# Optimization experiments

Hardware: AMD Instinct MI355X
Metric: run time of the kernel (lower is better)

Reference implementation:

```python
import jax, jax.numpy as jnp
import numpy as np

N_FFT = 4096
HOP = 1024
HALF = N_FFT // 2  # 2048; also number of freq bins is HALF+1 = 2049


def _make_kernels():
    # Periodic hann window, matching torch.hann_window(N) default (periodic=True)
    n = np.arange(N_FFT, dtype=np.float32)
    window = 0.5 * (1.0 - np.cos(2.0 * np.pi * n / N_FFT))
    freqs = np.arange(HALF + 1, dtype=np.float32)[:, None]  # [K,1]
    omega = 2.0 * np.pi * freqs * n[None, :] / N_FFT        # [K, n_fft]
    scale = np.float32(1.0 / np.sqrt(N_FFT))                # normalized=True
    cos_k = (np.cos(omega) * window[None, :] * scale).astype(np.float32)
    sin_k = (-np.sin(omega) * window[None, :] * scale).astype(np.float32)
    return jnp.asarray(cos_k), jnp.asarray(sin_k)


def setup_inputs() -> dict:
    key = jax.random.key(0)
    x = jax.random.normal(key, (32, 1, 441000), dtype=jnp.float32)
    cos_kernel, sin_kernel = _make_kernels()  # each [2049, 4096]
    return {"x": x, "cos_kernel": cos_kernel, "sin_kernel": sin_kernel}


def reference(x, cos_kernel, sin_kernel):
    # center=True: reflect-pad half_n_fft on each side of the time axis
    xp = jnp.pad(x, ((0, 0), (0, 0), (HALF, HALF)), mode='reflect')  # [B,1,L]
    L = xp.shape[-1]
    num_frames = (L - N_FFT) // HOP + 1
    # Frame extraction (equivalent to stride-HOP conv1d with width-N_FFT kernels)
    idx = HOP * jnp.arange(num_frames)[:, None] + jnp.arange(N_FFT)[None, :]  # [F, n_fft]
    frames = xp[:, 0, :][:, idx]  # [B, F, n_fft]
    real = jnp.einsum('bfn,kn->bkf', frames, cos_kernel)  # [B, 2049, F]
    imag = jnp.einsum('bfn,kn->bkf', frames, sin_kernel)  # [B, 2049, F]
    return jnp.stack((real, imag), axis=-1)  # [B, 2049, F, 2]
```

## Files before the change

kernel.cpp:

```cpp
#include <hip/hip_runtime.h>
#include <math.h>

#define NFFT  4096
#define MHALF 2048
#define HOPSZ 1024
#define LX    441000
#define NB    32
#define NF    431
#define NK    2049
#define NFPB  8
#define FBLK  54
#define NWG3  (NB * FBLK)
#define CH3   (NWG3 / 8)

#define SW(A) ((A) ^ (((A) >> 4) & 0xF))
#define WAVESYNC() do { asm volatile("s_waitcnt lgkmcnt(0)" ::: "memory"); \
                        __builtin_amdgcn_sched_barrier(0); } while (0)

typedef __fp16 half2v __attribute__((ext_vector_type(2)));

__device__ __forceinline__ float2 cadd(float2 a, float2 b){ return make_float2(a.x+b.x, a.y+b.y); }
__device__ __forceinline__ float2 csub(float2 a, float2 b){ return make_float2(a.x-b.x, a.y-b.y); }
__device__ __forceinline__ float2 cmul(float2 a, float2 b){
  return make_float2(fmaf(a.x, b.x, -(a.y*b.y)), fmaf(a.x, b.y, a.y*b.x));
}
#define STH(ptr, idx, v) (ptr)[idx] = __builtin_amdgcn_cvt_pkrtz((v).x, (v).y)
__device__ __forceinline__ float2 ldh(const half2v* __restrict__ X, int idx) {
  half2v h = X[idx];
  return make_float2((float)h.x, (float)h.y);
}

__global__ void stft_init(float* __restrict__ ws) {
  int i = blockIdx.x * blockDim.x + threadIdx.x;
  const double PI = 3.14159265358979323846;
  if (i < 4096) {
    double w = 0.5 * (1.0 - cos(2.0 * PI * (double)i / 4096.0)) * (1.0 / 64.0);
    ws[i] = (float)w;
  }
  if (i < 1024) {
    double a = -2.0 * PI * (double)i / 2048.0;
    ws[4096 + 2 * i]     = (float)cos(a);
    ws[4096 + 2 * i + 1] = (float)sin(a);
  }
  if (i < 2049) {
    double a = -2.0 * PI * (double)i / 4096.0;
    ws[6144 + 2 * i]     = (float)cos(a);
    ws[6144 + 2 * i + 1] = (float)sin(a);
  }
}

template<int S>
__device__ __forceinline__ void bf8(half2v* __restrict__ X,
                                    const float2* __restrict__ twg,
                                    int j, const float2* a) {
  const int q = j & (S - 1);
  const int t = j - q;
  float2 t0 = cadd(a[0], a[4]), t1 = csub(a[0], a[4]);
  float2 t2 = cadd(a[2], a[6]), t3 = csub(a[2], a[6]);
  float2 t4 = cadd(a[1], a[5]), t5 = csub(a[1], a[5]);
  float2 t6 = cadd(a[3], a[7]), t7 = csub(a[3], a[7]);

  const float K = 0.70710678118654752f;
  float2 wt5  = make_float2(K * (t5.x + t5.y), K * (t5.y - t5.x));
  float2 w3t7 = make_float2(K * (t7.y - t7.x), -K * (t7.x + t7.y));
  float2 wt7  = make_float2(K * (t7.x + t7.y), K * (t7.y - t7.x));
  float2 w3t5 = make_float2(K * (t5.y - t5.x), -K * (t5.x + t5.y));

  float2 e0 = cadd(t0, t2), e1 = csub(t0, t2);
  float2 f0 = cadd(t4, t6), f1 = csub(t4, t6);
  float2 B0 = cadd(e0, f0);
  float2 B4 = csub(e0, f0);
  float2 B2 = make_float2(e1.x + f1.y, e1.y - f1.x);
  float2 B6 = make_float2(e1.x - f1.y, e1.y + f1.x);
  float2 g0 = make_float2(t1.x + t3.y, t1.y - t3.x);
  float2 g1 = make_float2(t1.x - t3.y, t1.y + t3.x);
  float2 h0 = cadd(wt5, w3t7);
  float2 h1 = cadd(wt7, w3t5);
  float2 B1 = cadd(g0, h0);
  float2 B5 = csub(g0, h0);
  float2 B3 = cadd(g1, h1);
  float2 B7 = csub(g1, h1);

  float2 w1 = twg[t];
  float2 w2 = cmul(w1, w1);
  float2 w3 = cmul(w2, w1);
  float2 w4 = cmul(w2, w2);
  float2 w5 = cmul(w3, w2);
  float2 w6 = cmul(w3, w3);
  float2 w7 = cmul(w4, w3);

  const int o = q + 8 * t;
  STH(X, SW(o), B0);
  { float2 v = cmul(w1, B1); STH(X, SW(o + S),     v); }
  { float2 v = cmul(w2, B2); STH(X, SW(o + 2 * S), v); }
  { float2 v = cmul(w3, B3); STH(X, SW(o + 3 * S), v); }
  { float2 v = cmul(w4, B4); STH(X, SW(o + 4 * S), v); }
  { float2 v = cmul(w5, B5); STH(X, SW(o + 5 * S), v); }
  { float2 v = cmul(w6, B6); STH(X, SW(o + 6 * S), v); }
  { float2 v = cmul(w7, B7); STH(X, SW(o + 7 * S), v); }
}

__global__ __launch_bounds__(512) void stft_fft(const float* __restrict__ x,
                                                const float* __restrict__ ws,
                                                float* __restrict__ out) {
  __shared__ half2v fbuf[NFPB * 2048];

  const int tid = threadIdx.x;
  const int wid = (blockIdx.x & 7) * CH3 + (blockIdx.x >> 3);
  const int b  = wid / FBLK;
  const int fb = wid - b * FBLK;
  const int f0 = fb * NFPB;
  const int wv = tid >> 6;
  const int l  = tid & 63;
  const int f  = f0 + wv;

  const float*  win  = ws;
  const float2* winv = (const float2*)ws;
  const float2* twg  = (const float2*)(ws + 4096);
  const float2* tw4  = (const float2*)(ws + 6144);
  const float* xb = x + (size_t)b * LX;

  if (f < NF) {
    half2v* __restrict__ sl = &fbuf[wv * 2048];
    const int base = f * HOPSZ - MHALF;

    float2 a[4][8];
    if (base >= 0 && base + NFFT <= LX) {
      const float2* xv = (const float2*)(xb + base);
#pragma unroll
      for (int r = 0; r < 4; ++r) {
        const int j = l + (r << 6);
#pragma unroll
        for (int m = 0; m < 8; ++m) {
          const int idx = j + (m << 8);
          float2 v = xv[idx];
          float2 w = winv[idx];
          a[r][m] = make_float2(v.x * w.x, v.y * w.y);
        }
      }
    } else {
#pragma unroll
      for (int r = 0; r < 4; ++r) {
        const int j = l + (r << 6);
#pragma unroll
        for (int m = 0; m < 8; ++m) {
          const int idx = j + (m << 8);
          int s0 = base + 2 * idx;
          int s1 = s0 + 1;
          s0 = (s0 < 0) ? -s0 : ((s0 >= LX) ? (2 * LX - 2 - s0) : s0);
          s1 = (s1 < 0) ? -s1 : ((s1 >= LX) ? (2 * LX - 2 - s1) : s1);
          a[r][m] = make_float2(xb[s0] * win[2 * idx], xb[s1] * win[2 * idx + 1]);
        }
      }
    }
#pragma unroll
    for (int r = 0; r < 4; ++r) bf8<1>(sl, twg, l + (r << 6), a[r]);
    WAVESYNC();

#pragma unroll
    for (int r = 0; r < 4; ++r) {
      const int j = l + (r << 6);
#pragma unroll
      for (int m = 0; m < 8; ++m) a[r][m] = ldh(sl, SW(j + (m << 8)));
    }
    WAVESYNC();
#pragma unroll
    for (int r = 0; r < 4; ++r) bf8<8>(sl, twg, l + (r << 6), a[r]);
    WAVESYNC();

#pragma unroll
    for (int r = 0; r < 4; ++r) {
      const int j = l + (r << 6);
#pragma unroll
      for (int m = 0; m < 8; ++m) a[r][m] = ldh(sl, SW(j + (m << 8)));
    }
    WAVESYNC();
#pragma unroll
    for (int r = 0; r < 4; ++r) bf8<64>(sl, twg, l + (r << 6), a[r]);
    WAVESYNC();

#pragma unroll
    for (int r = 0; r < 8; ++r) {
      const int j = l + (r << 6);
      float2 c0 = ldh(sl, SW(j));
      float2 c1 = ldh(sl, SW(j + 512));
      float2 c2 = ldh(sl, SW(j + 1024));
      float2 c3 = ldh(sl, SW(j + 1536));
      float2 e0 = cadd(c0, c2), e1 = csub(c0, c2);
      float2 o0 = cadd(c1, c3), o1 = csub(c1, c3);
      { float2 v = cadd(e0, o0);                          STH(sl, SW(j),        v); }
      { float2 v = make_float2(e1.x + o1.y, e1.y - o1.x); STH(sl, SW(j + 512),  v); }
      { float2 v = csub(e0, o0);                          STH(sl, SW(j + 1024), v); }
      { float2 v = make_float2(e1.x - o1.y, e1.y + o1.x); STH(sl, SW(j + 1536), v); }
    }
  }
  __syncthreads();

  float2* __restrict__ op = (float2*)out;
  const size_t obB = (size_t)b * NK * NF;
  const int s  = tid & 7;
  const int kk = tid >> 3;
  const int fS = f0 + s;
  const bool act = (fS < NF);
  const half2v* __restrict__ sl = &fbuf[s * 2048];
#pragma unroll 4
  for (int it = 0; it < 32; ++it) {
    const int k  = kk + (it << 6);
    const int km = (2048 - k) & 2047;
    float2 zk = ldh(sl, SW(k));
    float2 zm = ldh(sl, SW(km));
    float xex = 0.5f * (zk.x + zm.x);
    float xey = 0.5f * (zk.y - zm.y);
    float xox = 0.5f * (zk.y + zm.y);
    float xoy = 0.5f * (zm.x - zk.x);
    float2 w = tw4[k];
    if (act)
      op[obB + (size_t)k * NF + fS] =
          make_float2(xex + w.x * xox - w.y * xoy, xey + w.x * xoy + w.y * xox);
  }
  if (tid < 8 && act) {
    float2 z0 = ldh(sl, 0);
    op[obB + (size_t)2048 * NF + fS] = make_float2(z0.x - z0.y, 0.0f);
  }
}

extern "C" void kernel_launch(void* const* d_in, const int* in_sizes, int n_in,
                              void* d_out, int out_size, void* d_ws, size_t ws_size,
                              hipStream_t stream) {
  const float* x = (const float*)d_in[0];
  float* ws = (float*)d_ws;
  float* out = (float*)d_out;
  stft_init<<<16, 256, 0, stream>>>(ws);
  stft_fft<<<NWG3, 512, 0, stream>>>(x, ws, out);
}
```

Baseline: 140.4 us.

## Merge last FFT stages into a register radix-32 pass and exploit conjugate symmetry

Replaces the final radix-8 LDS pass and the radix-4 pass with a single in-register radix-32 step: 32 values are loaded once, a radix-4 butterfly runs, then radix-8 DFTs with compile-time twiddles. This removes one LDS round trip and its wave syncs. The post-processing loop now uses the Hermitian symmetry of the real-FFT split, so each iteration writes bins k and 2048-k and the loop count is halved. A per-wave XOR offset is also added to the LDS addressing, likely to spread bank conflicts across waves. The radix-32 pass needs more registers, and the special-case handling of bins 0, 1024 and 2048 changes.

```diff
diff --git a/kernel.cpp b/kernel.cpp
--- a/kernel.cpp
+++ b/kernel.cpp
@@ -30,6 +30,29 @@
   return make_float2((float)h.x, (float)h.y);
 }
 
+constexpr float W32C[22] = {
+  1.0f, 0.98078528040323f, 0.92387953251129f, 0.83146961230255f, 0.70710678118655f,
+  0.55557023301960f, 0.38268343236509f, 0.19509032201613f, 0.0f, -0.19509032201613f,
+  -0.38268343236509f, -0.55557023301960f, -0.70710678118655f, -0.83146961230255f,
+  -0.92387953251129f, -0.98078528040323f, -1.0f, -0.98078528040323f,
+  -0.92387953251129f, -0.83146961230255f, -0.70710678118655f, -0.55557023301960f };
+constexpr float W32S[22] = {
+  0.0f, 0.19509032201613f, 0.38268343236509f, 0.55557023301960f, 0.70710678118655f,
+  0.83146961230255f, 0.92387953251129f, 0.98078528040323f, 1.0f, 0.98078528040323f,
+  0.92387953251129f, 0.83146961230255f, 0.70710678118655f, 0.55557023301960f,
+  0.38268343236509f, 0.19509032201613f, 0.0f, -0.19509032201613f,
+  -0.38268343236509f, -0.55557023301960f, -0.70710678118655f, -0.83146961230255f };
+
+template<int N> __device__ __forceinline__ float2 w32m(float2 z) {
+  if constexpr (N == 0) { return z; }
+  else if constexpr (N == 8) { return make_float2(z.y, -z.x); }
+  else {
+    constexpr float c = W32C[N];
+    constexpr float s = W32S[N];
+    return make_float2(fmaf(z.x, c, z.y * s), fmaf(z.y, c, -(z.x * s)));
+  }
+}
+
 __global__ void stft_init(float* __restrict__ ws) {
   int i = blockIdx.x * blockDim.x + threadIdx.x;
   const double PI = 3.14159265358979323846;
@@ -49,38 +72,40 @@
   }
 }
 
-template<int S>
-__device__ __forceinline__ void bf8(half2v* __restrict__ X,
-                                    const float2* __restrict__ twg,
-                                    int j, const float2* a) {
-  const int q = j & (S - 1);
-  const int t = j - q;
+__device__ __forceinline__ void dft8(const float2* a, float2* B) {
   float2 t0 = cadd(a[0], a[4]), t1 = csub(a[0], a[4]);
   float2 t2 = cadd(a[2], a[6]), t3 = csub(a[2], a[6]);
   float2 t4 = cadd(a[1], a[5]), t5 = csub(a[1], a[5]);
   float2 t6 = cadd(a[3], a[7]), t7 = csub(a[3], a[7]);
-
   const float K = 0.70710678118654752f;
   float2 wt5  = make_float2(K * (t5.x + t5.y), K * (t5.y - t5.x));
   float2 w3t7 = make_float2(K * (t7.y - t7.x), -K * (t7.x + t7.y));
   float2 wt7  = make_float2(K * (t7.x + t7.y), K * (t7.y - t7.x));
   float2 w3t5 = make_float2(K * (t5.y - t5.x), -K * (t5.x + t5.y));
-
   float2 e0 = cadd(t0, t2), e1 = csub(t0, t2);
   float2 f0 = cadd(t4, t6), f1 = csub(t4, t6);
-  float2 B0 = cadd(e0, f0);
-  float2 B4 = csub(e0, f0);
-  float2 B2 = make_float2(e1.x + f1.y, e1.y - f1.x);
-  float2 B6 = make_float2(e1.x - f1.y, e1.y + f1.x);
+  B[0] = cadd(e0, f0);
+  B[4] = csub(e0, f0);
+  B[2] = make_float2(e1.x + f1.y, e1.y - f1.x);
+  B[6] = make_float2(e1.x - f1.y, e1.y + f1.x);
   float2 g0 = make_float2(t1.x + t3.y, t1.y - t3.x);
   float2 g1 = make_float2(t1.x - t3.y, t1.y + t3.x);
   float2 h0 = cadd(wt5, w3t7);
   float2 h1 = cadd(wt7, w3t5);
-  float2 B1 = cadd(g0, h0);
-  float2 B5 = csub(g0, h0);
-  float2 B3 = cadd(g1, h1);
-  float2 B7 = csub(g1, h1);
-
+  B[1] = cadd(g0, h0);
+  B[5] = csub(g0, h0);
+  B[3] = cadd(g1, h1);
+  B[7] = csub(g1, h1);
+}
+
+template<int S>
+__device__ __forceinline__ void bf8(half2v* __restrict__ X, int sxor,
+                                    const float2* __restrict__ twg,
+                                    int j, const float2* a) {
+  const int q = j & (S - 1);
+  const int t = j - q;
+  float2 B[8];
+  dft8(a, B);
   float2 w1 = twg[t];
   float2 w2 = cmul(w1, w1);
   float2 w3 = cmul(w2, w1);
@@ -88,17 +113,37 @@
   float2 w5 = cmul(w3, w2);
   float2 w6 = cmul(w3, w3);
   float2 w7 = cmul(w4, w3);
-
   const int o = q + 8 * t;
-  STH(X, SW(o), B0);
-  { float2 v = cmul(w1, B1); STH(X, SW(o + S),     v); }
-  { float2 v = cmul(w2, B2); STH(X, SW(o + 2 * S), v); }
-  { float2 v = cmul(w3, B3); STH(X, SW(o + 3 * S), v); }
-  { float2 v = cmul(w4, B4); STH(X, SW(o + 4 * S), v); }
-  { float2 v = cmul(w5, B5); STH(X, SW(o + 5 * S), v); }
-  { float2 v = cmul(w6, B6); STH(X, SW(o + 6 * S), v); }
-  { float2 v = cmul(w7, B7); STH(X, SW(o + 7 * S), v); }
-}
+  STH(X, SW(o) ^ sxor, B[0]);
+  { float2 v = cmul(w1, B[1]); STH(X, SW(o + S)     ^ sxor, v); }
+  { float2 v = cmul(w2, B[2]); STH(X, SW(o + 2 * S) ^ sxor, v); }
+  { float2 v = cmul(w3, B[3]); STH(X, SW(o + 3 * S) ^ sxor, v); }
+  { float2 v = cmul(w4, B[4]); STH(X, SW(o + 4 * S) ^ sxor, v); }
+  { float2 v = cmul(w5, B[5]); STH(X, SW(o + 5 * S) ^ sxor, v); }
+  { float2 v = cmul(w6, B[6]); STH(X, SW(o + 6 * S) ^ sxor, v); }
+  { float2 v = cmul(w7, B[7]); STH(X, SW(o + 7 * S) ^ sxor, v); }
+}
+
+#define VBLK(V) do {                                                  \
+    float2 tt[8], BB[8];                                              \
+    tt[0] = d[8*(V)+0];                                               \
+    tt[1] = w32m<1*(V)>(d[8*(V)+1]);                                  \
+    tt[2] = w32m<2*(V)>(d[8*(V)+2]);                                  \
+    tt[3] = w32m<3*(V)>(d[8*(V)+3]);                                  \
+    tt[4] = w32m<4*(V)>(d[8*(V)+4]);                                  \
+    tt[5] = w32m<5*(V)>(d[8*(V)+5]);                                  \
+    tt[6] = w32m<6*(V)>(d[8*(V)+6]);                                  \
+    tt[7] = w32m<7*(V)>(d[8*(V)+7]);                                  \
+    dft8(tt, BB);                                                     \
+    STH(sl, SW(l + (((V) +  0) << 6)) ^ sxor, BB[0]);                 \
+    STH(sl, SW(l + (((V) +  4) << 6)) ^ sxor, BB[1]);                 \
+    STH(sl, SW(l + (((V) +  8) << 6)) ^ sxor, BB[2]);                 \
+    STH(sl, SW(l + (((V) + 12) << 6)) ^ sxor, BB[3]);                 \
+    STH(sl, SW(l + (((V) + 16) << 6)) ^ sxor, BB[4]);                 \
+    STH(sl, SW(l + (((V) + 20) << 6)) ^ sxor, BB[5]);                 \
+    STH(sl, SW(l + (((V) + 24) << 6)) ^ sxor, BB[6]);                 \
+    STH(sl, SW(l + (((V) + 28) << 6)) ^ sxor, BB[7]);                 \
+  } while (0)
 
 __global__ __launch_bounds__(512) void stft_fft(const float* __restrict__ x,
                                                 const float* __restrict__ ws,
@@ -122,6 +167,7 @@
 
   if (f < NF) {
     half2v* __restrict__ sl = &fbuf[wv * 2048];
+    const int sxor = wv << 2;
     const int base = f * HOPSZ - MHALF;
 
     float2 a[4][8];
@@ -154,45 +200,34 @@
       }
     }
 #pragma unroll
-    for (int r = 0; r < 4; ++r) bf8<1>(sl, twg, l + (r << 6), a[r]);
+    for (int r = 0; r < 4; ++r) bf8<1>(sl, sxor, twg, l + (r << 6), a[r]);
     WAVESYNC();
 
 #pragma unroll
     for (int r = 0; r < 4; ++r) {
       const int j = l + (r << 6);
 #pragma unroll
-      for (int m = 0; m < 8; ++m) a[r][m] = ldh(sl, SW(j + (m << 8)));
+      for (int m = 0; m < 8; ++m) a[r][m] = ldh(sl, SW(j + (m << 8)) ^ sxor);
     }
     WAVESYNC();
 #pragma unroll
-    for (int r = 0; r < 4; ++r) bf8<8>(sl, twg, l + (r << 6), a[r]);
+    for (int r = 0; r < 4; ++r) bf8<8>(sl, sxor, twg, l + (r << 6), a[r]);
     WAVESYNC();
 
-#pragma unroll
-    for (int r = 0; r < 4; ++r) {
-      const int j = l + (r << 6);
-#pragma unroll
-      for (int m = 0; m < 8; ++m) a[r][m] = ldh(sl, SW(j + (m << 8)));
-    }
-    WAVESYNC();
-#pragma unroll
-    for (int r = 0; r < 4; ++r) bf8<64>(sl, twg, l + (r << 6), a[r]);
-    WAVESYNC();
-
-#pragma unroll
-    for (int r = 0; r < 8; ++r) {
-      const int j = l + (r << 6);
-      float2 c0 = ldh(sl, SW(j));
-      float2 c1 = ldh(sl, SW(j + 512));
-      float2 c2 = ldh(sl, SW(j + 1024));
-      float2 c3 = ldh(sl, SW(j + 1536));
-      float2 e0 = cadd(c0, c2), e1 = csub(c0, c2);
-      float2 o0 = cadd(c1, c3), o1 = csub(c1, c3);
-      { float2 v = cadd(e0, o0);                          STH(sl, SW(j),        v); }
-      { float2 v = make_float2(e1.x + o1.y, e1.y - o1.x); STH(sl, SW(j + 512),  v); }
-      { float2 v = csub(e0, o0);                          STH(sl, SW(j + 1024), v); }
-      { float2 v = make_float2(e1.x - o1.y, e1.y + o1.x); STH(sl, SW(j + 1536), v); }
-    }
+    float2 d[32];
+#pragma unroll
+    for (int m = 0; m < 32; ++m) d[m] = ldh(sl, SW(l + (m << 6)) ^ sxor);
+#pragma unroll
+    for (int m1 = 0; m1 < 8; ++m1) {
+      float2 p0 = d[m1], p1 = d[m1 + 8], p2 = d[m1 + 16], p3 = d[m1 + 24];
+      float2 e0 = cadd(p0, p2), e1 = csub(p0, p2);
+      float2 o0 = cadd(p1, p3), o1 = csub(p1, p3);
+      d[m1]      = cadd(e0, o0);
+      d[m1 + 8]  = make_float2(e1.x + o1.y, e1.y - o1.x);
+      d[m1 + 16] = csub(e0, o0);
+      d[m1 + 24] = make_float2(e1.x - o1.y, e1.y + o1.x);
+    }
+    VBLK(0); VBLK(1); VBLK(2); VBLK(3);
   }
   __syncthreads();
 
@@ -202,25 +237,30 @@
   const int kk = tid >> 3;
   const int fS = f0 + s;
   const bool act = (fS < NF);
-  const half2v* __restrict__ sl = &fbuf[s * 2048];
+  const half2v* __restrict__ sl2 = &fbuf[s * 2048];
+  const int sx2 = s << 2;
 #pragma unroll 4
-  for (int it = 0; it < 32; ++it) {
+  for (int it = 0; it < 16; ++it) {
     const int k  = kk + (it << 6);
     const int km = (2048 - k) & 2047;
-    float2 zk = ldh(sl, SW(k));
-    float2 zm = ldh(sl, SW(km));
+    float2 zk = ldh(sl2, SW(k)  ^ sx2);
+    float2 zm = ldh(sl2, SW(km) ^ sx2);
     float xex = 0.5f * (zk.x + zm.x);
     float xey = 0.5f * (zk.y - zm.y);
     float xox = 0.5f * (zk.y + zm.y);
     float xoy = 0.5f * (zm.x - zk.x);
     float2 w = tw4[k];
-    if (act)
-      op[obB + (size_t)k * NF + fS] =
-          make_float2(xex + w.x * xox - w.y * xoy, xey + w.x * xoy + w.y * xox);
-  }
-  if (tid < 8 && act) {
-    float2 z0 = ldh(sl, 0);
-    op[obB + (size_t)2048 * NF + fS] = make_float2(z0.x - z0.y, 0.0f);
+    float tx = w.x * xox - w.y * xoy;
+    float ty = w.x * xoy + w.y * xox;
+    if (act) {
+      op[obB + (size_t)k * NF + fS]          = make_float2(xex + tx,  xey + ty);
+      op[obB + (size_t)(2048 - k) * NF + fS] = make_float2(xex - tx, -xey + ty);
+    }
+  }
+  if (tid < 8 && (f0 + tid) < NF) {
+    const half2v* slt = &fbuf[tid * 2048];
+    float2 zq = ldh(slt, SW(1024) ^ (tid << 2));
+    op[obB + (size_t)1024 * NF + (f0 + tid)] = make_float2(zq.x, -zq.y);
   }
 }
 
```

Measured after the change: 137.3 us. -2.2%, faster.
